# Kernel optimization log

Hardware: AMD Instinct MI355X
Metric: run time of the kernel (lower is better)

Reference implementation:

```python
import jax, jax.numpy as jnp
import numpy as np

NUM_TOKENS = 16384
HIDDEN = 4096
NUM_EXPERTS = 64
TOP_K = 8


def setup_inputs() -> dict:
    key = jax.random.key(0)
    k1, k2 = jax.random.split(key)
    x = jax.random.normal(k1, (NUM_TOKENS, HIDDEN), dtype=jnp.float32)
    # nn.Linear default init scale ~ 1/sqrt(fan_in); keep logits well-scaled
    gate_w = jax.random.normal(k2, (NUM_EXPERTS, HIDDEN), dtype=jnp.float32) / jnp.sqrt(jnp.float32(HIDDEN))
    gate_b = jnp.zeros((NUM_EXPERTS,), dtype=jnp.float32)
    return {"x": x, "gate_w": gate_w, "gate_b": gate_b}


def reference(x, gate_w, gate_b):
    # gate linear: (T, H) @ (H, E) + (E,) -> (T, E)
    g = jnp.einsum("th,eh->te", x, gate_w) + gate_b
    # top-k over experts (sorted descending, like torch.topk)
    top_vals, top_idx = jax.lax.top_k(g, TOP_K)  # (T, K) each
    # softmax over the k selected logits
    expert_weights = jax.nn.softmax(top_vals, axis=-1)
    return expert_weights, top_idx
```

## Files before the change

kernel.cpp:

```cpp
#include <hip/hip_runtime.h>
#include <math.h>


#define NT 16384
#define HID 4096
#define NE 64
#define TOPK 8
#define BT 32
#define CK 64
#define NCH (HID / CK)
#define SK 72
#define LG_S 65
#define MARGIN 2.5e-4f

typedef __attribute__((ext_vector_type(8))) short bf16x8;
typedef __attribute__((ext_vector_type(4))) float f32x4;

__global__ __launch_bounds__(256, 2)
void gating_kernel(const float* __restrict__ x,
                   const float* __restrict__ gw,
                   const float* __restrict__ gb,
                   float* __restrict__ out) {
    __shared__ unsigned short sx_hi[BT * SK], sx_lo[BT * SK];
    __shared__ unsigned short sw_hi[NE * SK], sw_lo[NE * SK];
    __shared__ float lg[BT * LG_S];
    __shared__ float thr9s[BT];
    __shared__ int flags[BT], flist[BT], fcnt;

    const int tid  = threadIdx.x;
    const int ln   = tid & 63;
    const int wv   = __builtin_amdgcn_readfirstlane(tid >> 6);
    const int tok0 = blockIdx.x * BT;
    const int tb   = (wv & 1) * 16;
    const int eb   = (wv >> 1) * 32;
    const int mr   = ln & 15;
    const int q    = ln >> 4;

    f32x4 acc0 = {0.f, 0.f, 0.f, 0.f};
    f32x4 acc1 = {0.f, 0.f, 0.f, 0.f};

    float4 px[2], pw[4];
#pragma unroll
    for (int j = 0; j < 2; j++) {
        int fl = j * 256 + tid, r = fl >> 4, c = (fl & 15) << 2;
        px[j] = *(const float4*)(x + (size_t)(tok0 + r) * HID + c);
    }
#pragma unroll
    for (int j = 0; j < 4; j++) {
        int fl = j * 256 + tid, r = fl >> 4, c = (fl & 15) << 2;
        pw[j] = *(const float4*)(gw + (size_t)r * HID + c);
    }

    for (int ch = 0; ch < NCH; ch++) {
        __syncthreads();
#pragma unroll
        for (int j = 0; j < 2; j++) {
            int fl = j * 256 + tid, r = fl >> 4, c = (fl & 15) << 2;
            float4 v = px[j];
            uint u0 = __float_as_uint(v.x), u1 = __float_as_uint(v.y);
            uint u2 = __float_as_uint(v.z), u3 = __float_as_uint(v.w);
            ushort4 hi = make_ushort4(u0 >> 16, u1 >> 16, u2 >> 16, u3 >> 16);
            float l0 = v.x - __uint_as_float(u0 & 0xFFFF0000u);
            float l1 = v.y - __uint_as_float(u1 & 0xFFFF0000u);
            float l2 = v.z - __uint_as_float(u2 & 0xFFFF0000u);
            float l3 = v.w - __uint_as_float(u3 & 0xFFFF0000u);
            ushort4 lo = make_ushort4(__float_as_uint(l0) >> 16, __float_as_uint(l1) >> 16,
                                      __float_as_uint(l2) >> 16, __float_as_uint(l3) >> 16);
            *(ushort4*)&sx_hi[r * SK + c] = hi;
            *(ushort4*)&sx_lo[r * SK + c] = lo;
        }
#pragma unroll
        for (int j = 0; j < 4; j++) {
            int fl = j * 256 + tid, r = fl >> 4, c = (fl & 15) << 2;
            float4 v = pw[j];
            uint u0 = __float_as_uint(v.x), u1 = __float_as_uint(v.y);
            uint u2 = __float_as_uint(v.z), u3 = __float_as_uint(v.w);
            ushort4 hi = make_ushort4(u0 >> 16, u1 >> 16, u2 >> 16, u3 >> 16);
            float l0 = v.x - __uint_as_float(u0 & 0xFFFF0000u);
            float l1 = v.y - __uint_as_float(u1 & 0xFFFF0000u);
            float l2 = v.z - __uint_as_float(u2 & 0xFFFF0000u);
            float l3 = v.w - __uint_as_float(u3 & 0xFFFF0000u);
            ushort4 lo = make_ushort4(__float_as_uint(l0) >> 16, __float_as_uint(l1) >> 16,
                                      __float_as_uint(l2) >> 16, __float_as_uint(l3) >> 16);
            *(ushort4*)&sw_hi[r * SK + c] = hi;
            *(ushort4*)&sw_lo[r * SK + c] = lo;
        }
        __syncthreads();

        if (ch + 1 < NCH) {
            const int k0 = (ch + 1) * CK;
#pragma unroll
            for (int j = 0; j < 2; j++) {
                int fl = j * 256 + tid, r = fl >> 4, c = (fl & 15) << 2;
                px[j] = *(const float4*)(x + (size_t)(tok0 + r) * HID + k0 + c);
            }
#pragma unroll
            for (int j = 0; j < 4; j++) {
                int fl = j * 256 + tid, r = fl >> 4, c = (fl & 15) << 2;
                pw[j] = *(const float4*)(gw + (size_t)r * HID + k0 + c);
            }
        }

        const int aof  = (tb + mr) * SK + q * 8;
        const int b0of = (eb + mr) * SK + q * 8;
        const int b1of = (eb + 16 + mr) * SK + q * 8;
#pragma unroll
        for (int s = 0; s < 2; s++) {
            const int o = s * 32;
            bf16x8 ah  = *(const bf16x8*)&sx_hi[aof + o];
            bf16x8 al  = *(const bf16x8*)&sx_lo[aof + o];
            bf16x8 b0h = *(const bf16x8*)&sw_hi[b0of + o];
            bf16x8 b0l = *(const bf16x8*)&sw_lo[b0of + o];
            bf16x8 b1h = *(const bf16x8*)&sw_hi[b1of + o];
            bf16x8 b1l = *(const bf16x8*)&sw_lo[b1of + o];
            acc0 = __builtin_amdgcn_mfma_f32_16x16x32_bf16(ah, b0h, acc0, 0, 0, 0);
            acc1 = __builtin_amdgcn_mfma_f32_16x16x32_bf16(ah, b1h, acc1, 0, 0, 0);
            acc0 = __builtin_amdgcn_mfma_f32_16x16x32_bf16(ah, b0l, acc0, 0, 0, 0);
            acc1 = __builtin_amdgcn_mfma_f32_16x16x32_bf16(ah, b1l, acc1, 0, 0, 0);
            acc0 = __builtin_amdgcn_mfma_f32_16x16x32_bf16(al, b0h, acc0, 0, 0, 0);
            acc1 = __builtin_amdgcn_mfma_f32_16x16x32_bf16(al, b1h, acc1, 0, 0, 0);
            acc0 = __builtin_amdgcn_mfma_f32_16x16x32_bf16(al, b0l, acc0, 0, 0, 0);
            acc1 = __builtin_amdgcn_mfma_f32_16x16x32_bf16(al, b1l, acc1, 0, 0, 0);
        }
    }

    __syncthreads();
    {
        int e0 = eb + mr, e1 = eb + 16 + mr;
        float bb0 = gb[e0], bb1 = gb[e1];
#pragma unroll
        for (int i = 0; i < 4; i++) {
            int t = tb + q * 4 + i;
            lg[t * LG_S + e0] = acc0[i] + bb0;
            lg[t * LG_S + e1] = acc1[i] + bb1;
        }
    }
    if (tid == 0) fcnt = 0;
    __syncthreads();

    float vals[9];
    int idxs[9];
    int myflag = 0;
    if (ln < 8) {
        int t = wv * 8 + ln;
        const float* row = &lg[t * LG_S];
        unsigned long long sel = 0ull;
#pragma unroll
        for (int kk = 0; kk < 9; kk++) {
            float bv = -1e30f;
            int bi = 0;
            for (int e = 0; e < NE; e++) {
                bool valid = !((sel >> e) & 1ull);
                float v = row[e];
                bool take = valid && (v > bv);
                bv = take ? v : bv;
                bi = take ? e : bi;
            }
            sel |= 1ull << bi;
            vals[kk] = bv;
            idxs[kk] = bi;
        }
        float mg = 1e30f;
#pragma unroll
        for (int kk = 0; kk < 8; kk++) {
            float g = vals[kk] - vals[kk + 1];
            mg = (g < mg) ? g : mg;
        }
        myflag = (mg < MARGIN) ? 1 : 0;
        flags[t] = myflag;
        thr9s[t] = vals[8];
        if (!myflag) {
            float mx = vals[0], ex[TOPK], s = 0.f;
#pragma unroll
            for (int k = 0; k < TOPK; k++) { ex[k] = expf(vals[k] - mx); s += ex[k]; }
            float inv = 1.0f / s;
            int gt = tok0 + t;
#pragma unroll
            for (int k = 0; k < TOPK; k++) {
                out[gt * TOPK + k] = ex[k] * inv;
                out[NT * TOPK + gt * TOPK + k] = (float)idxs[k];
            }
        }
    }
    __syncthreads();

    if (tid == 0) {
        int n = 0;
        for (int t = 0; t < BT; t++) if (flags[t]) flist[n++] = t;
        fcnt = n;
    }
    __syncthreads();

    for (int i = wv; i < fcnt; i += 4) {
        int t = flist[i];
        bool active = lg[t * LG_S + ln] >= thr9s[t] - MARGIN;
        double p0 = 0., p1 = 0., p2 = 0., p3 = 0.;
        if (active) {
            const float* xr = x + (size_t)(tok0 + t) * HID;
            const float* wr = gw + (size_t)ln * HID;
            for (int k = 0; k < HID; k += 4) {
                float4 a = *(const float4*)(xr + k);
                float4 b = *(const float4*)(wr + k);
                p0 = fma((double)a.x, (double)b.x, p0);
                p1 = fma((double)a.y, (double)b.y, p1);
                p2 = fma((double)a.z, (double)b.z, p2);
                p3 = fma((double)a.w, (double)b.w, p3);
            }
        }
        double base = active ? ((p0 + p1) + (p2 + p3) + (double)gb[ln]) : -1e18;
        double mv[TOPK];
        int mi[TOPK];
#pragma unroll
        for (int k = 0; k < TOPK; k++) {
            double v = base;
            int ii = ln;
#pragma unroll
            for (int off = 32; off >= 1; off >>= 1) {
                double ov = __shfl_xor(v, off);
                int oi = __shfl_xor(ii, off);
                if (ov > v || (ov == v && oi < ii)) { v = ov; ii = oi; }
            }
            mv[k] = v;
            mi[k] = ii;
            if (ln == ii) base = -1e18;
        }
        if (ln == 0) {
            double mx = mv[0];
            float ex[TOPK], s = 0.f;
#pragma unroll
            for (int k = 0; k < TOPK; k++) { ex[k] = expf((float)(mv[k] - mx)); s += ex[k]; }
            float inv = 1.0f / s;
            int gt = tok0 + t;
#pragma unroll
            for (int k = 0; k < TOPK; k++) {
                out[gt * TOPK + k] = ex[k] * inv;
                out[NT * TOPK + gt * TOPK + k] = (float)mi[k];
            }
        }
    }
}

extern "C" void kernel_launch(void* const* d_in, const int* in_sizes, int n_in,
                              void* d_out, int out_size, void* d_ws, size_t ws_size,
                              hipStream_t stream) {
    const float* x  = (const float*)d_in[0];
    const float* gw = (const float*)d_in[1];
    const float* gb = (const float*)d_in[2];
    float* out = (float*)d_out;

    dim3 grid(NT / BT);
    dim3 block(256);
    gating_kernel<<<grid, block, 0, stream>>>(x, gw, gb, out);
}
```

Measured before the change: 507.4 us.

## Drop LDS staging, load MFMA operands directly from global, presplit weights

```diff
diff --git a/kernel.cpp b/kernel.cpp
--- a/kernel.cpp
+++ b/kernel.cpp
@@ -6,23 +6,67 @@
 #define HID 4096
 #define NE 64
 #define TOPK 8
-#define BT 32
-#define CK 64
-#define NCH (HID / CK)
-#define SK 72
+#define BT 16
 #define LG_S 65
 #define MARGIN 2.5e-4f
 
 typedef __attribute__((ext_vector_type(8))) short bf16x8;
 typedef __attribute__((ext_vector_type(4))) float f32x4;
 
-__global__ __launch_bounds__(256, 2)
+union BF8 { unsigned int u[4]; bf16x8 v; };
+
+__device__ __forceinline__ unsigned int hi_pack(float a, float b) {
+    return __builtin_amdgcn_perm(__float_as_uint(b), __float_as_uint(a), 0x07060302u);
+}
+
+__device__ __forceinline__ float lo_of(float f) {
+    return f - __uint_as_float(__float_as_uint(f) & 0xFFFF0000u);
+}
+
+__device__ __forceinline__ bf16x8 pack_hi8(float4 a, float4 b) {
+    BF8 r;
+    r.u[0] = hi_pack(a.x, a.y);
+    r.u[1] = hi_pack(a.z, a.w);
+    r.u[2] = hi_pack(b.x, b.y);
+    r.u[3] = hi_pack(b.z, b.w);
+    return r.v;
+}
+
+__device__ __forceinline__ bf16x8 pack_lo8(float4 a, float4 b) {
+    BF8 r;
+    r.u[0] = hi_pack(lo_of(a.x), lo_of(a.y));
+    r.u[1] = hi_pack(lo_of(a.z), lo_of(a.w));
+    r.u[2] = hi_pack(lo_of(b.x), lo_of(b.y));
+    r.u[3] = hi_pack(lo_of(b.z), lo_of(b.w));
+    return r.v;
+}
+
+__global__ __launch_bounds__(256)
+void presplit_kernel(const float* __restrict__ gw,
+                     unsigned short* __restrict__ whi,
+                     unsigned short* __restrict__ wlo) {
+    int i = (blockIdx.x * 256 + threadIdx.x) * 4;
+    float4 v = *(const float4*)(gw + i);
+    ushort4 hi = make_ushort4((unsigned short)(__float_as_uint(v.x) >> 16),
+                              (unsigned short)(__float_as_uint(v.y) >> 16),
+                              (unsigned short)(__float_as_uint(v.z) >> 16),
+                              (unsigned short)(__float_as_uint(v.w) >> 16));
+    ushort4 lo = make_ushort4((unsigned short)(__float_as_uint(lo_of(v.x)) >> 16),
+                              (unsigned short)(__float_as_uint(lo_of(v.y)) >> 16),
+                              (unsigned short)(__float_as_uint(lo_of(v.z)) >> 16),
+                              (unsigned short)(__float_as_uint(lo_of(v.w)) >> 16));
+    *(ushort4*)(whi + i) = hi;
+    *(ushort4*)(wlo + i) = lo;
+}
+
+template <bool PS>
+__global__ __launch_bounds__(256, 4)
 void gating_kernel(const float* __restrict__ x,
                    const float* __restrict__ gw,
+                   const unsigned short* __restrict__ whi,
+                   const unsigned short* __restrict__ wlo,
                    const float* __restrict__ gb,
                    float* __restrict__ out) {
-    __shared__ unsigned short sx_hi[BT * SK], sx_lo[BT * SK];
-    __shared__ unsigned short sw_hi[NE * SK], sw_lo[NE * SK];
     __shared__ float lg[BT * LG_S];
     __shared__ float thr9s[BT];
     __shared__ int flags[BT], flist[BT], fcnt;
@@ -31,154 +75,125 @@
     const int ln   = tid & 63;
     const int wv   = __builtin_amdgcn_readfirstlane(tid >> 6);
     const int tok0 = blockIdx.x * BT;
-    const int tb   = (wv & 1) * 16;
-    const int eb   = (wv >> 1) * 32;
+    const int eb   = wv * 16;
     const int mr   = ln & 15;
     const int q    = ln >> 4;
 
-    f32x4 acc0 = {0.f, 0.f, 0.f, 0.f};
-    f32x4 acc1 = {0.f, 0.f, 0.f, 0.f};
-
-    float4 px[2], pw[4];
-#pragma unroll
-    for (int j = 0; j < 2; j++) {
-        int fl = j * 256 + tid, r = fl >> 4, c = (fl & 15) << 2;
-        px[j] = *(const float4*)(x + (size_t)(tok0 + r) * HID + c);
-    }
-#pragma unroll
-    for (int j = 0; j < 4; j++) {
-        int fl = j * 256 + tid, r = fl >> 4, c = (fl & 15) << 2;
-        pw[j] = *(const float4*)(gw + (size_t)r * HID + c);
-    }
-
-    for (int ch = 0; ch < NCH; ch++) {
-        __syncthreads();
-#pragma unroll
-        for (int j = 0; j < 2; j++) {
-            int fl = j * 256 + tid, r = fl >> 4, c = (fl & 15) << 2;
-            float4 v = px[j];
-            uint u0 = __float_as_uint(v.x), u1 = __float_as_uint(v.y);
-            uint u2 = __float_as_uint(v.z), u3 = __float_as_uint(v.w);
-            ushort4 hi = make_ushort4(u0 >> 16, u1 >> 16, u2 >> 16, u3 >> 16);
-            float l0 = v.x - __uint_as_float(u0 & 0xFFFF0000u);
-            float l1 = v.y - __uint_as_float(u1 & 0xFFFF0000u);
-            float l2 = v.z - __uint_as_float(u2 & 0xFFFF0000u);
-            float l3 = v.w - __uint_as_float(u3 & 0xFFFF0000u);
-            ushort4 lo = make_ushort4(__float_as_uint(l0) >> 16, __float_as_uint(l1) >> 16,
-                                      __float_as_uint(l2) >> 16, __float_as_uint(l3) >> 16);
-            *(ushort4*)&sx_hi[r * SK + c] = hi;
-            *(ushort4*)&sx_lo[r * SK + c] = lo;
-        }
-#pragma unroll
-        for (int j = 0; j < 4; j++) {
-            int fl = j * 256 + tid, r = fl >> 4, c = (fl & 15) << 2;
-            float4 v = pw[j];
-            uint u0 = __float_as_uint(v.x), u1 = __float_as_uint(v.y);
-            uint u2 = __float_as_uint(v.z), u3 = __float_as_uint(v.w);
-            ushort4 hi = make_ushort4(u0 >> 16, u1 >> 16, u2 >> 16, u3 >> 16);
-            float l0 = v.x - __uint_as_float(u0 & 0xFFFF0000u);
-            float l1 = v.y - __uint_as_float(u1 & 0xFFFF0000u);
-            float l2 = v.z - __uint_as_float(u2 & 0xFFFF0000u);
-            float l3 = v.w - __uint_as_float(u3 & 0xFFFF0000u);
-            ushort4 lo = make_ushort4(__float_as_uint(l0) >> 16, __float_as_uint(l1) >> 16,
-                                      __float_as_uint(l2) >> 16, __float_as_uint(l3) >> 16);
-            *(ushort4*)&sw_hi[r * SK + c] = hi;
-            *(ushort4*)&sw_lo[r * SK + c] = lo;
-        }
-        __syncthreads();
-
-        if (ch + 1 < NCH) {
-            const int k0 = (ch + 1) * CK;
-#pragma unroll
-            for (int j = 0; j < 2; j++) {
-                int fl = j * 256 + tid, r = fl >> 4, c = (fl & 15) << 2;
-                px[j] = *(const float4*)(x + (size_t)(tok0 + r) * HID + k0 + c);
-            }
-#pragma unroll
-            for (int j = 0; j < 4; j++) {
-                int fl = j * 256 + tid, r = fl >> 4, c = (fl & 15) << 2;
-                pw[j] = *(const float4*)(gw + (size_t)r * HID + k0 + c);
-            }
-        }
-
-        const int aof  = (tb + mr) * SK + q * 8;
-        const int b0of = (eb + mr) * SK + q * 8;
-        const int b1of = (eb + 16 + mr) * SK + q * 8;
-#pragma unroll
-        for (int s = 0; s < 2; s++) {
-            const int o = s * 32;
-            bf16x8 ah  = *(const bf16x8*)&sx_hi[aof + o];
-            bf16x8 al  = *(const bf16x8*)&sx_lo[aof + o];
-            bf16x8 b0h = *(const bf16x8*)&sw_hi[b0of + o];
-            bf16x8 b0l = *(const bf16x8*)&sw_lo[b0of + o];
-            bf16x8 b1h = *(const bf16x8*)&sw_hi[b1of + o];
-            bf16x8 b1l = *(const bf16x8*)&sw_lo[b1of + o];
-            acc0 = __builtin_amdgcn_mfma_f32_16x16x32_bf16(ah, b0h, acc0, 0, 0, 0);
-            acc1 = __builtin_amdgcn_mfma_f32_16x16x32_bf16(ah, b1h, acc1, 0, 0, 0);
-            acc0 = __builtin_amdgcn_mfma_f32_16x16x32_bf16(ah, b0l, acc0, 0, 0, 0);
-            acc1 = __builtin_amdgcn_mfma_f32_16x16x32_bf16(ah, b1l, acc1, 0, 0, 0);
-            acc0 = __builtin_amdgcn_mfma_f32_16x16x32_bf16(al, b0h, acc0, 0, 0, 0);
-            acc1 = __builtin_amdgcn_mfma_f32_16x16x32_bf16(al, b1h, acc1, 0, 0, 0);
-            acc0 = __builtin_amdgcn_mfma_f32_16x16x32_bf16(al, b0l, acc0, 0, 0, 0);
-            acc1 = __builtin_amdgcn_mfma_f32_16x16x32_bf16(al, b1l, acc1, 0, 0, 0);
-        }
-    }
-
-    __syncthreads();
+    const float* a_p = x + (size_t)(tok0 + mr) * HID + q * 8;
+    const float*          b_p = gw  + (size_t)(eb + mr) * HID + q * 8;
+    const unsigned short* h_p = whi + (size_t)(eb + mr) * HID + q * 8;
+    const unsigned short* l_p = wlo + (size_t)(eb + mr) * HID + q * 8;
+
+    f32x4 acc = {0.f, 0.f, 0.f, 0.f};
+
+    float4 pa[2][2];
+    bf16x8 ph[2], pl[2];
+    float4 pb[2][2];
+
+    pa[0][0] = *(const float4*)(a_p + 0);
+    pa[0][1] = *(const float4*)(a_p + 4);
+    if constexpr (PS) {
+        ph[0] = *(const bf16x8*)(h_p + 0);
+        pl[0] = *(const bf16x8*)(l_p + 0);
+    } else {
+        pb[0][0] = *(const float4*)(b_p + 0);
+        pb[0][1] = *(const float4*)(b_p + 4);
+    }
+
+    for (int g = 0; g < 8; ++g) {
+#pragma unroll
+        for (int u = 0; u < 16; ++u) {
+            const int slot = u & 1;
+            const int ns   = slot ^ 1;
+            if (g * 16 + u + 1 < 128) {
+                const int off = (u + 1) * 32;
+                pa[ns][0] = *(const float4*)(a_p + off);
+                pa[ns][1] = *(const float4*)(a_p + off + 4);
+                if constexpr (PS) {
+                    ph[ns] = *(const bf16x8*)(h_p + off);
+                    pl[ns] = *(const bf16x8*)(l_p + off);
+                } else {
+                    pb[ns][0] = *(const float4*)(b_p + off);
+                    pb[ns][1] = *(const float4*)(b_p + off + 4);
+                }
+            }
+            bf16x8 ah = pack_hi8(pa[slot][0], pa[slot][1]);
+            bf16x8 al = pack_lo8(pa[slot][0], pa[slot][1]);
+            bf16x8 bh, bl;
+            if constexpr (PS) {
+                bh = ph[slot]; bl = pl[slot];
+            } else {
+                bh = pack_hi8(pb[slot][0], pb[slot][1]);
+                bl = pack_lo8(pb[slot][0], pb[slot][1]);
+            }
+            acc = __builtin_amdgcn_mfma_f32_16x16x32_bf16(ah, bh, acc, 0, 0, 0);
+            acc = __builtin_amdgcn_mfma_f32_16x16x32_bf16(ah, bl, acc, 0, 0, 0);
+            acc = __builtin_amdgcn_mfma_f32_16x16x32_bf16(al, bh, acc, 0, 0, 0);
+            acc = __builtin_amdgcn_mfma_f32_16x16x32_bf16(al, bl, acc, 0, 0, 0);
+        }
+        a_p += 512; h_p += 512; l_p += 512; b_p += 512;
+        __builtin_amdgcn_s_barrier();
+    }
+
     {
-        int e0 = eb + mr, e1 = eb + 16 + mr;
-        float bb0 = gb[e0], bb1 = gb[e1];
-#pragma unroll
-        for (int i = 0; i < 4; i++) {
-            int t = tb + q * 4 + i;
-            lg[t * LG_S + e0] = acc0[i] + bb0;
-            lg[t * LG_S + e1] = acc1[i] + bb1;
-        }
+        const int e0 = eb + mr;
+        const float bb = gb[e0];
+#pragma unroll
+        for (int i = 0; i < 4; ++i)
+            lg[(q * 4 + i) * LG_S + e0] = acc[i] + bb;
     }
     if (tid == 0) fcnt = 0;
     __syncthreads();
 
-    float vals[9];
-    int idxs[9];
-    int myflag = 0;
-    if (ln < 8) {
-        int t = wv * 8 + ln;
-        const float* row = &lg[t * LG_S];
-        unsigned long long sel = 0ull;
-#pragma unroll
-        for (int kk = 0; kk < 9; kk++) {
-            float bv = -1e30f;
-            int bi = 0;
-            for (int e = 0; e < NE; e++) {
-                bool valid = !((sel >> e) & 1ull);
-                float v = row[e];
-                bool take = valid && (v > bv);
-                bv = take ? v : bv;
-                bi = take ? e : bi;
-            }
-            sel |= 1ull << bi;
-            vals[kk] = bv;
-            idxs[kk] = bi;
-        }
+    const int t = wv * 4 + q;
+    float v0 = lg[t * LG_S + mr * 4 + 0];
+    float v1 = lg[t * LG_S + mr * 4 + 1];
+    float v2 = lg[t * LG_S + mr * 4 + 2];
+    float v3 = lg[t * LG_S + mr * 4 + 3];
+    float vals9[9];
+    int idx9[9];
+#pragma unroll
+    for (int kk = 0; kk < 9; ++kk) {
+        float bv = v0; int bj = 0;
+        if (v1 > bv) { bv = v1; bj = 1; }
+        if (v2 > bv) { bv = v2; bj = 2; }
+        if (v3 > bv) { bv = v3; bj = 3; }
+        int be = (mr << 2) | bj;
+#pragma unroll
+        for (int off = 1; off <= 8; off <<= 1) {
+            float ov = __shfl_xor(bv, off);
+            int   oe = __shfl_xor(be, off);
+            if (ov > bv || (ov == bv && oe < be)) { bv = ov; be = oe; }
+        }
+        vals9[kk] = bv; idx9[kk] = be;
+        if (kk < 8 && (be >> 2) == mr) {
+            int j = be & 3;
+            v0 = (j == 0) ? -1e30f : v0;
+            v1 = (j == 1) ? -1e30f : v1;
+            v2 = (j == 2) ? -1e30f : v2;
+            v3 = (j == 3) ? -1e30f : v3;
+        }
+    }
+    if (mr == 0) {
         float mg = 1e30f;
 #pragma unroll
         for (int kk = 0; kk < 8; kk++) {
-            float g = vals[kk] - vals[kk + 1];
-            mg = (g < mg) ? g : mg;
-        }
-        myflag = (mg < MARGIN) ? 1 : 0;
-        flags[t] = myflag;
-        thr9s[t] = vals[8];
-        if (!myflag) {
-            float mx = vals[0], ex[TOPK], s = 0.f;
-#pragma unroll
-            for (int k = 0; k < TOPK; k++) { ex[k] = expf(vals[k] - mx); s += ex[k]; }
+            float gp = vals9[kk] - vals9[kk + 1];
+            mg = (gp < mg) ? gp : mg;
+        }
+        int fl = (mg < MARGIN) ? 1 : 0;
+        flags[t] = fl;
+        thr9s[t] = vals9[8];
+        if (!fl) {
+            float mx = vals9[0], ex[TOPK], s = 0.f;
+#pragma unroll
+            for (int k = 0; k < TOPK; k++) { ex[k] = expf(vals9[k] - mx); s += ex[k]; }
             float inv = 1.0f / s;
             int gt = tok0 + t;
 #pragma unroll
             for (int k = 0; k < TOPK; k++) {
                 out[gt * TOPK + k] = ex[k] * inv;
-                out[NT * TOPK + gt * TOPK + k] = (float)idxs[k];
+                out[NT * TOPK + gt * TOPK + k] = (float)idx9[k];
             }
         }
     }
@@ -186,18 +201,19 @@
 
     if (tid == 0) {
         int n = 0;
-        for (int t = 0; t < BT; t++) if (flags[t]) flist[n++] = t;
+        for (int tt = 0; tt < BT; tt++) if (flags[tt]) flist[n++] = tt;
         fcnt = n;
     }
     __syncthreads();
 
-    for (int i = wv; i < fcnt; i += 4) {
-        int t = flist[i];
-        bool active = lg[t * LG_S + ln] >= thr9s[t] - MARGIN;
+    for (int i2 = wv; i2 < fcnt; i2 += 4) {
+        int tt = flist[i2];
+        bool active = lg[tt * LG_S + ln] >= thr9s[tt] - MARGIN;
         double p0 = 0., p1 = 0., p2 = 0., p3 = 0.;
         if (active) {
-            const float* xr = x + (size_t)(tok0 + t) * HID;
+            const float* xr = x + (size_t)(tok0 + tt) * HID;
             const float* wr = gw + (size_t)ln * HID;
+#pragma unroll 4
             for (int k = 0; k < HID; k += 4) {
                 float4 a = *(const float4*)(xr + k);
                 float4 b = *(const float4*)(wr + k);
@@ -230,7 +246,7 @@
 #pragma unroll
             for (int k = 0; k < TOPK; k++) { ex[k] = expf((float)(mv[k] - mx)); s += ex[k]; }
             float inv = 1.0f / s;
-            int gt = tok0 + t;
+            int gt = tok0 + tt;
 #pragma unroll
             for (int k = 0; k < TOPK; k++) {
                 out[gt * TOPK + k] = ex[k] * inv;
@@ -248,7 +264,14 @@
     const float* gb = (const float*)d_in[2];
     float* out = (float*)d_out;
 
-    dim3 grid(NT / BT);
-    dim3 block(256);
-    gating_kernel<<<grid, block, 0, stream>>>(x, gw, gb, out);
-}
+    const size_t ws_need = (size_t)NE * HID * 4;
+    bool ps = (d_ws != nullptr) && (ws_size >= ws_need);
+    if (ps) {
+        unsigned short* whi = (unsigned short*)d_ws;
+        unsigned short* wlo = whi + (size_t)NE * HID;
+        presplit_kernel<<<dim3(NE * HID / 1024), dim3(256), 0, stream>>>(gw, whi, wlo);
+        gating_kernel<true><<<dim3(NT / BT), dim3(256), 0, stream>>>(x, gw, whi, wlo, gb, out);
+    } else {
+        gating_kernel<false><<<dim3(NT / BT), dim3(256), 0, stream>>>(x, gw, nullptr, nullptr, gb, out);
+    }
+}
```

After: 619.7 us. 1.22x slower.
